# Optimization experiments

Measured on AMD Instinct MI355X. Metric: run time of the kernel, lower is better.

The kernel has to match this reference:

```python
import jax, jax.numpy as jnp
import numpy as np
from jax import lax

B, T, D, L, OUT, HORIZON, TSLOTS, NDAY = 512, 24, 1024, 2, 325, 12, 288, 7


def setup_inputs() -> dict:
    key = jax.random.key(0)
    ks = jax.random.split(key, 20)
    s_d = 1.0 / np.sqrt(D)
    s_o = 1.0 / np.sqrt(OUT)
    inp = {
        'data': jax.random.normal(ks[0], (B, T, OUT), jnp.float32),
        'time': jax.random.randint(ks[1], (B, T), 0, TSLOTS),
        'weekday': jax.random.randint(ks[2], (B,), 0, NDAY),
        # embedding params
        'w_data': jax.random.normal(ks[3], (OUT, D), jnp.float32) * s_o,
        'b_data': jnp.zeros((D,), jnp.float32),
        'time_table': jax.random.normal(ks[4], (TSLOTS, D), jnp.float32) * 0.02,
        'day_table': jax.random.normal(ks[5], (NDAY, D), jnp.float32) * 0.02,
        # encoder GRU (input_size == hidden_size == D for all layers)
        'enc_Wih': jax.random.uniform(ks[6], (L, 3 * D, D), jnp.float32, -s_d, s_d),
        'enc_Whh': jax.random.uniform(ks[7], (L, 3 * D, D), jnp.float32, -s_d, s_d),
        'enc_bih': jax.random.uniform(ks[8], (L, 3 * D), jnp.float32, -s_d, s_d),
        'enc_bhh': jax.random.uniform(ks[9], (L, 3 * D), jnp.float32, -s_d, s_d),
        # decoder GRU
        'dec_Wih': jax.random.uniform(ks[10], (L, 3 * D, D), jnp.float32, -s_d, s_d),
        'dec_Whh': jax.random.uniform(ks[11], (L, 3 * D, D), jnp.float32, -s_d, s_d),
        'dec_bih': jax.random.uniform(ks[12], (L, 3 * D), jnp.float32, -s_d, s_d),
        'dec_bhh': jax.random.uniform(ks[13], (L, 3 * D), jnp.float32, -s_d, s_d),
        # decoder output MLP (dropout=0 -> linear)
        'w_mlp': jax.random.uniform(ks[14], (D, OUT), jnp.float32, -s_d, s_d),
        'b_mlp': jnp.zeros((OUT,), jnp.float32),
    }
    return inp


def _gru_cell(h, x, Wih, Whh, bih, bhh):
    # torch GRUCell math. h,x: [B,D]
    gx = x @ Wih.T + bih            # [B,3D]
    gh = h @ Whh.T + bhh
    xr, xz, xn = jnp.split(gx, 3, axis=-1)
    hr, hz, hn = jnp.split(gh, 3, axis=-1)
    r = jax.nn.sigmoid(xr + hr)
    z = jax.nn.sigmoid(xz + hz)
    n = jnp.tanh(xn + r * hn)
    return (1.0 - z) * n + z * h


def _gru_layer(x, h0, Wih, Whh, bih, bhh):
    # x: [B,S,D] -> outputs [B,S,D], final h [B,D]
    def step(h, xt):
        h2 = _gru_cell(h, xt, Wih, Whh, bih, bhh)
        return h2, h2
    hT, ys = lax.scan(step, h0, jnp.moveaxis(x, 1, 0))
    return jnp.moveaxis(ys, 0, 1), hT


def reference(data, time, weekday, w_data, b_data, time_table, day_table,
              enc_Wih, enc_Whh, enc_bih, enc_bhh,
              dec_Wih, dec_Whh, dec_bih, dec_bhh, w_mlp, b_mlp):
    def embed(d, t, wd):  # d:[B,S,OUT] t:[B,S] wd:[B]
        return (d @ w_data + b_data
                + time_table[t % TSLOTS]
                + day_table[wd][:, None, :])

    # ---- encoder over history (all but last step) ----
    x = embed(data[:, :-1], time[:, :-1], weekday)  # [B,T-1,D]
    h_layers = []
    for l in range(L):
        x, hl = _gru_layer(x, jnp.zeros((B, D), x.dtype),
                           enc_Wih[l], enc_Whh[l], enc_bih[l], enc_bhh[l])
        h_layers.append(hl)
    hidden = jnp.stack(h_layers)  # [L,B,D]

    def dec_step(carry, _):
        hidden, data_i, time_i = carry  # [L,B,D], [B,1,OUT], [B,1]
        xi = embed(data_i, time_i, weekday)[:, 0]  # [B,D]
        new_h = []
        h_in = xi
        for l in range(L):
            hl = _gru_cell(hidden[l], h_in, dec_Wih[l], dec_Whh[l],
                           dec_bih[l], dec_bhh[l])
            new_h.append(hl)
            h_in = hl
        res = h_in @ w_mlp + b_mlp              # [B,OUT]
        out_i = data_i[:, 0] + res
        data_next = data_i[:, 0] + lax.stop_gradient(res)
        return (jnp.stack(new_h), data_next[:, None], time_i + 1), out_i

    carry0 = (hidden, data[:, -1:], time[:, -1:])
    _, outs = lax.scan(dec_step, carry0, None, length=HORIZON)  # [H,B,OUT]
    return jnp.moveaxis(outs, 0, 1)  # [B,H,OUT]
```

## Files before the change

### kernel.cpp

```cpp
#include <hip/hip_runtime.h>
#include <math.h>

#define B_ 512
#define T_ 24
#define TM1 23
#define D_ 1024
#define OUT_ 325
#define HORIZON_ 12

typedef unsigned short ushort_t;
typedef __attribute__((ext_vector_type(8))) short bf16x8;
typedef __attribute__((ext_vector_type(4))) float f32x4;

#define MFMA16(a, b, c) __builtin_amdgcn_mfma_f32_16x16x32_bf16((a), (b), (c), 0, 0, 0)

__device__ __forceinline__ ushort_t f2b(float f) {
  union { float f; unsigned u; } v; v.f = f;
  unsigned r = (v.u + 0x7fffu + ((v.u >> 16) & 1u)) >> 16;
  return (ushort_t)r;
}
__device__ __forceinline__ float b2f(ushort_t s) {
  union { unsigned u; float f; } v; v.u = ((unsigned)s) << 16;
  return v.f;
}

__device__ __forceinline__ size_t pidx16(int m, int k, int K) {
  return (((size_t)(m >> 4) * (K >> 5) + (k >> 5)) * 64
          + ((m & 15) + (((k >> 3) & 3) << 4))) * 8 + (k & 7);
}

#define GLOAD16(src, dst) \
  __builtin_amdgcn_global_load_lds((const __attribute__((address_space(1))) void*)(src), \
                                   (__attribute__((address_space(3))) void*)(dst), 16, 0, 0)

__global__ __launch_bounds__(256) void enc_diag(
    int k,
    const ushort_t* __restrict__ Hp0, const float* __restrict__ Hf0,
    float* __restrict__ Hf0o, ushort_t* __restrict__ Hp0o,
    const ushort_t* __restrict__ Whh0, const float* __restrict__ bhh0,
    const ushort_t* __restrict__ GXbuf, ushort_t* __restrict__ Y0p,
    const ushort_t* __restrict__ Hp1, const float* __restrict__ Hf1,
    float* __restrict__ Hf1o, ushort_t* __restrict__ Hp1o,
    const ushort_t* __restrict__ Wih1, const ushort_t* __restrict__ Whh1,
    const float* __restrict__ bih1, const float* __restrict__ bhh1)
{
  __shared__ ushort_t lds[2][16 * 512];
  const int tid = threadIdx.x, lane = tid & 63, w = tid >> 6;
  const int bid = blockIdx.x;
  const int z = bid >> 9, bx = (bid >> 5) & 15, by = bid & 31;
  const int wm = w >> 1, wn = w & 1;
  const int d = by * 32 + wn * 16 + (lane & 15);

  if (z == 0) {
    if (k >= TM1) return;
    const ushort_t* GXslot = GXbuf + (size_t)k * 512 * 3072;
    ushort_t* Seqp = Y0p + (size_t)k * 512 * 1024;
    f32x4 acc[3] = {};
    auto stage = [&](int buf, int kb) {
      #pragma unroll
      for (int r = 0; r < 2; ++r) {
        int s = w * 2 + r;
        const ushort_t* src;
        if (s < 2) src = Hp0 + ((size_t)(((bx * 32 + s * 16) >> 4) * 32 + kb)) * 512 + lane * 8;
        else { int g = (s - 2) >> 1, hf = (s - 2) & 1;
          src = Whh0 + ((size_t)((g * 64 + by * 2 + hf) * 32 + kb)) * 512 + lane * 8; }
        GLOAD16(src, &lds[buf][s * 512 + lane * 8]);
      }
    };
    stage(0, 0); __syncthreads();
    int cur = 0;
    for (int kb = 0; kb < 32; ++kb) {
      if (kb + 1 < 32) stage(cur ^ 1, kb + 1);
      const ushort_t* L = lds[cur];
      bf16x8 a = *(const bf16x8*)(L + wm * 512 + lane * 8);
      #pragma unroll
      for (int g = 0; g < 3; ++g) {
        bf16x8 b = *(const bf16x8*)(L + (2 + g * 2 + wn) * 512 + lane * 8);
        acc[g] = MFMA16(a, b, acc[g]);
      }
      __syncthreads(); cur ^= 1;
    }
    const float bh_r = bhh0[d], bh_z = bhh0[D_ + d], bh_n = bhh0[2 * D_ + d];
    #pragma unroll
    for (int q = 0; q < 4; ++q) {
      int m = bx * 32 + wm * 16 + ((lane >> 4) << 2) + q;
      const ushort_t* gxp = GXslot + (size_t)m * 3072 + d;
      float gx_r = b2f(gxp[0]), gx_z = b2f(gxp[D_]), gx_n = b2f(gxp[2 * D_]);
      float rr = 1.f / (1.f + __expf(-(gx_r + acc[0][q] + bh_r)));
      float zz = 1.f / (1.f + __expf(-(gx_z + acc[1][q] + bh_z)));
      float nn = tanhf(gx_n + rr * (acc[2][q] + bh_n));
      float h = Hf0[(size_t)m * D_ + d];
      float hnew = (1.f - zz) * nn + zz * h;
      Hf0o[(size_t)m * D_ + d] = hnew;
      ushort_t hb = f2b(hnew);
      size_t pi = pidx16(m, d, D_);
      Hp0o[pi] = hb; Seqp[pi] = hb;
    }
  } else {
    if (k < 1) return;
    const ushort_t* Xp_ = Y0p + (size_t)(k - 1) * 512 * 1024;
    f32x4 accx[3] = {}, acch[3] = {};
    auto stage = [&](int buf, int kb) {
      #pragma unroll
      for (int r = 0; r < 4; ++r) {
        int s = w * 4 + r;
        const ushort_t* src;
        if (s < 2) src = Xp_ + ((size_t)(((bx * 32 + s * 16) >> 4) * 32 + kb)) * 512 + lane * 8;
        else if (s < 4) src = Hp1 + ((size_t)(((bx * 32 + (s - 2) * 16) >> 4) * 32 + kb)) * 512 + lane * 8;
        else if (s < 10) { int g = (s - 4) >> 1, hf = (s - 4) & 1;
          src = Wih1 + ((size_t)((g * 64 + by * 2 + hf) * 32 + kb)) * 512 + lane * 8; }
        else { int g = (s - 10) >> 1, hf = (s - 10) & 1;
          src = Whh1 + ((size_t)((g * 64 + by * 2 + hf) * 32 + kb)) * 512 + lane * 8; }
        GLOAD16(src, &lds[buf][s * 512 + lane * 8]);
      }
    };
    stage(0, 0); __syncthreads();
    int cur = 0;
    for (int kb = 0; kb < 32; ++kb) {
      if (kb + 1 < 32) stage(cur ^ 1, kb + 1);
      const ushort_t* L = lds[cur];
      bf16x8 ax = *(const bf16x8*)(L + (0 + wm) * 512 + lane * 8);
      bf16x8 ah = *(const bf16x8*)(L + (2 + wm) * 512 + lane * 8);
      #pragma unroll
      for (int g = 0; g < 3; ++g) {
        bf16x8 bxw = *(const bf16x8*)(L + (4 + g * 2 + wn) * 512 + lane * 8);
        bf16x8 bhw = *(const bf16x8*)(L + (10 + g * 2 + wn) * 512 + lane * 8);
        accx[g] = MFMA16(ax, bxw, accx[g]);
        acch[g] = MFMA16(ah, bhw, acch[g]);
      }
      __syncthreads(); cur ^= 1;
    }
    const float bi_r = bih1[d], bi_z = bih1[D_ + d], bi_n = bih1[2 * D_ + d];
    const float bh_r = bhh1[d], bh_z = bhh1[D_ + d], bh_n = bhh1[2 * D_ + d];
    #pragma unroll
    for (int q = 0; q < 4; ++q) {
      int m = bx * 32 + wm * 16 + ((lane >> 4) << 2) + q;
      float rr = 1.f / (1.f + __expf(-(accx[0][q] + bi_r + acch[0][q] + bh_r)));
      float zz = 1.f / (1.f + __expf(-(accx[1][q] + bi_z + acch[1][q] + bh_z)));
      float nn = tanhf(accx[2][q] + bi_n + rr * (acch[2][q] + bh_n));
      float h = Hf1[(size_t)m * D_ + d];
      float hnew = (1.f - zz) * nn + zz * h;
      Hf1o[(size_t)m * D_ + d] = hnew;
      Hp1o[pidx16(m, d, D_)] = f2b(hnew);
    }
  }
}

__global__ __launch_bounds__(256) void dec_cell0(
    const ushort_t* __restrict__ DCp, const ushort_t* __restrict__ Hp,
    const float* __restrict__ Hf,
    const ushort_t* __restrict__ W0dp, const ushort_t* __restrict__ Whh0,
    const float* __restrict__ bhh0,
    const float* __restrict__ CTt, const float* __restrict__ CBd,
    const int* __restrict__ timev, int step,
    float* __restrict__ Hf_out, ushort_t* __restrict__ Hp_out)
{
  __shared__ ushort_t lds[2][16 * 512];
  const int tid = threadIdx.x, lane = tid & 63, w = tid >> 6;
  const int bid = blockIdx.x;
  const int bx = bid >> 5, by = bid & 31;
  const int wm = w >> 1, wn = w & 1;
  const int d = by * 32 + wn * 16 + (lane & 15);
  f32x4 accx[3] = {}, acch[3] = {};

  auto stage_h = [&](int buf, int kb) {
    #pragma unroll
    for (int r = 0; r < 2; ++r) {
      int s = (w == 0) ? (2 + r) : (8 + w * 2 + r);
      const ushort_t* src;
      if (s < 4) src = Hp + ((size_t)(((bx * 32 + (s - 2) * 16) >> 4) * 32 + kb)) * 512 + lane * 8;
      else { int g = (s - 10) >> 1, hf = (s - 10) & 1;
        src = Whh0 + ((size_t)((g * 64 + by * 2 + hf) * 32 + kb)) * 512 + lane * 8; }
      GLOAD16(src, &lds[buf][s * 512 + lane * 8]);
    }
  };
  auto stage_x = [&](int buf, int kb) {
    #pragma unroll
    for (int r = 0; r < 2; ++r) {
      int s = (w == 0) ? r : (2 + w * 2 + r);
      const ushort_t* src;
      if (s < 2) src = DCp + ((size_t)(((bx * 32 + s * 16) >> 4) * 11 + kb)) * 512 + lane * 8;
      else { int g = (s - 4) >> 1, hf = (s - 4) & 1;
        src = W0dp + ((size_t)((g * 64 + by * 2 + hf) * 11 + kb)) * 512 + lane * 8; }
      GLOAD16(src, &lds[buf][s * 512 + lane * 8]);
    }
  };

  stage_h(0, 0); stage_x(0, 0);
  __syncthreads();
  int cur = 0;
  for (int kb = 0; kb < 32; ++kb) {
    if (kb + 1 < 32) {
      stage_h(cur ^ 1, kb + 1);
      if (kb + 1 < 11) stage_x(cur ^ 1, kb + 1);
    }
    const ushort_t* L = lds[cur];
    bf16x8 ah = *(const bf16x8*)(L + (2 + wm) * 512 + lane * 8);
    if (kb < 11) {
      bf16x8 ax = *(const bf16x8*)(L + (0 + wm) * 512 + lane * 8);
      #pragma unroll
      for (int g = 0; g < 3; ++g) {
        bf16x8 bxw = *(const bf16x8*)(L + (4 + g * 2 + wn) * 512 + lane * 8);
        accx[g] = MFMA16(ax, bxw, accx[g]);
      }
    }
    #pragma unroll
    for (int g = 0; g < 3; ++g) {
      bf16x8 bhw = *(const bf16x8*)(L + (10 + g * 2 + wn) * 512 + lane * 8);
      acch[g] = MFMA16(ah, bhw, acch[g]);
    }
    __syncthreads(); cur ^= 1;
  }

  const float bh_r = bhh0[d], bh_z = bhh0[D_ + d], bh_n = bhh0[2 * D_ + d];
  #pragma unroll
  for (int q = 0; q < 4; ++q) {
    int m = bx * 32 + wm * 16 + ((lane >> 4) << 2) + q;
    int ti = (timev[m * T_ + (T_ - 1)] + step) % 288;
    const float* ctt = CTt + (size_t)ti * 3072;
    const float* cb  = CBd + (size_t)m * 3072;
    float gx_r = accx[0][q] + ctt[d] + cb[d];
    float gx_z = accx[1][q] + ctt[D_ + d] + cb[D_ + d];
    float gx_n = accx[2][q] + ctt[2 * D_ + d] + cb[2 * D_ + d];
    float rr = 1.f / (1.f + __expf(-(gx_r + acch[0][q] + bh_r)));
    float zz = 1.f / (1.f + __expf(-(gx_z + acch[1][q] + bh_z)));
    float nn = tanhf(gx_n + rr * (acch[2][q] + bh_n));
    float h = Hf[(size_t)m * D_ + d];
    float hnew = (1.f - zz) * nn + zz * h;
    Hf_out[(size_t)m * D_ + d] = hnew;
    Hp_out[pidx16(m, d, D_)] = f2b(hnew);
  }
}

__global__ __launch_bounds__(256) void gru_cell32(
    const ushort_t* __restrict__ Xp_, const ushort_t* __restrict__ Hp,
    const float* __restrict__ Hf,
    const ushort_t* __restrict__ Wih_l, const ushort_t* __restrict__ Whh_l,
    const float* __restrict__ bih_l, const float* __restrict__ bhh_l,
    float* __restrict__ Hf_out, ushort_t* __restrict__ Hp_out)
{
  __shared__ ushort_t lds[2][16 * 512];
  const int tid = threadIdx.x, lane = tid & 63, w = tid >> 6;
  const int bid = blockIdx.x;
  const int bx = bid >> 5, by = bid & 31;
  const int wm = w >> 1, wn = w & 1;
  const int d = by * 32 + wn * 16 + (lane & 15);
  f32x4 accx[3] = {}, acch[3] = {};

  auto stage = [&](int buf, int kb) {
    #pragma unroll
    for (int r = 0; r < 4; ++r) {
      int s = w * 4 + r;
      const ushort_t* src;
      if (s < 2) src = Xp_ + ((size_t)(((bx * 32 + s * 16) >> 4) * 32 + kb)) * 512 + lane * 8;
      else if (s < 4) src = Hp + ((size_t)(((bx * 32 + (s - 2) * 16) >> 4) * 32 + kb)) * 512 + lane * 8;
      else if (s < 10) { int g = (s - 4) >> 1, hf = (s - 4) & 1;
        src = Wih_l + ((size_t)((g * 64 + by * 2 + hf) * 32 + kb)) * 512 + lane * 8; }
      else { int g = (s - 10) >> 1, hf = (s - 10) & 1;
        src = Whh_l + ((size_t)((g * 64 + by * 2 + hf) * 32 + kb)) * 512 + lane * 8; }
      GLOAD16(src, &lds[buf][s * 512 + lane * 8]);
    }
  };

  stage(0, 0); __syncthreads();
  int cur = 0;
  for (int kb = 0; kb < 32; ++kb) {
    if (kb + 1 < 32) stage(cur ^ 1, kb + 1);
    const ushort_t* L = lds[cur];
    bf16x8 ax = *(const bf16x8*)(L + (0 + wm) * 512 + lane * 8);
    bf16x8 ah = *(const bf16x8*)(L + (2 + wm) * 512 + lane * 8);
    #pragma unroll
    for (int g = 0; g < 3; ++g) {
      bf16x8 bxw = *(const bf16x8*)(L + (4 + g * 2 + wn) * 512 + lane * 8);
      bf16x8 bhw = *(const bf16x8*)(L + (10 + g * 2 + wn) * 512 + lane * 8);
      accx[g] = MFMA16(ax, bxw, accx[g]);
      acch[g] = MFMA16(ah, bhw, acch[g]);
    }
    __syncthreads(); cur ^= 1;
  }

  const float bi_r = bih_l[d], bi_z = bih_l[D_ + d], bi_n = bih_l[2 * D_ + d];
  const float bh_r = bhh_l[d], bh_z = bhh_l[D_ + d], bh_n = bhh_l[2 * D_ + d];
  #pragma unroll
  for (int q = 0; q < 4; ++q) {
    int m = bx * 32 + wm * 16 + ((lane >> 4) << 2) + q;
    float rr = 1.f / (1.f + __expf(-(accx[0][q] + bi_r + acch[0][q] + bh_r)));
    float zz = 1.f / (1.f + __expf(-(accx[1][q] + bi_z + acch[1][q] + bh_z)));
    float nn = tanhf(accx[2][q] + bi_n + rr * (acch[2][q] + bh_n));
    float h = Hf[(size_t)m * D_ + d];
    float hnew = (1.f - zz) * nn + zz * h;
    Hf_out[(size_t)m * D_ + d] = hnew;
    Hp_out[pidx16(m, d, D_)] = f2b(hnew);
  }
}

__global__ __launch_bounds__(256) void gemm_gx0_enc(
    const ushort_t* __restrict__ Ap, const ushort_t* __restrict__ W0p,
    const float* __restrict__ CTt, const float* __restrict__ CBe,
    const int* __restrict__ timev,
    ushort_t* __restrict__ GX)
{
  __shared__ ushort_t lds[2][16 * 512];
  const int tid = threadIdx.x, lane = tid & 63, w = tid >> 6;
  const int bx = blockIdx.x, by = blockIdx.y;
  const int wm = w >> 1, wn = w & 1;
  f32x4 acc[4][4] = {};

  auto stage = [&](int buf, int kb) {
    #pragma unroll
    for (int r = 0; r < 4; ++r) {
      int s = r * 4 + w;
      const ushort_t* src = (s < 8)
          ? Ap  + ((size_t)((bx * 8 + s) * 11 + kb)) * 512 + lane * 8
          : W0p + ((size_t)((by * 8 + (s - 8)) * 11 + kb)) * 512 + lane * 8;
      GLOAD16(src, &lds[buf][s * 512 + lane * 8]);
    }
  };

  stage(0, 0); __syncthreads();
  int cur = 0;
  for (int kb = 0; kb < 11; ++kb) {
    if (kb + 1 < 11) stage(cur ^ 1, kb + 1);
    const ushort_t* L = lds[cur];
    bf16x8 af[4], bf[4];
    #pragma unroll
    for (int f = 0; f < 4; ++f) {
      af[f] = *(const bf16x8*)(L + (wm * 4 + f) * 512 + lane * 8);
      bf[f] = *(const bf16x8*)(L + (8 + wn * 4 + f) * 512 + lane * 8);
    }
    #pragma unroll
    for (int fm = 0; fm < 4; ++fm)
      #pragma unroll
      for (int fn = 0; fn < 4; ++fn)
        acc[fm][fn] = MFMA16(af[fm], bf[fn], acc[fm][fn]);
    __syncthreads(); cur ^= 1;
  }

  float* fl = (float*)&lds[0][0];
  for (int fm = 0; fm < 4; ++fm) {
    #pragma unroll
    for (int q = 0; q < 4; ++q)
      #pragma unroll
      for (int fn = 0; fn < 4; ++fn)
        fl[(wm * 16 + ((lane >> 4) << 2) + q) * 132 + wn * 64 + fn * 16 + (lane & 15)]
            = acc[fm][fn][q];
    __syncthreads();
    #pragma unroll
    for (int it = 0; it < 2; ++it) {
      int idx = it * 256 + tid;
      int ml = idx >> 4, n0 = (idx & 15) * 8;
      int m = bx * 128 + (ml >> 4) * 64 + fm * 16 + (ml & 15);
      int b = m / 23, t = m - b * 23;
      int ti = timev[b * T_ + t] % 288;
      const float* ctt = CTt + (size_t)ti * 3072 + by * 128 + n0;
      const float* cb  = CBe + (size_t)b * 3072 + by * 128 + n0;
      const float* fr  = fl + ml * 132 + n0;
      bf16x8 o;
      #pragma unroll
      for (int j = 0; j < 8; ++j) o[j] = f2b(fr[j] + ctt[j] + cb[j]);
      *(bf16x8*)(GX + ((size_t)t * 512 + b) * 3072 + by * 128 + n0) = o;
    }
    __syncthreads();
  }
}

template<int EPI>
__global__ __launch_bounds__(256) void gemm64(
    const ushort_t* __restrict__ Ap, const ushort_t* __restrict__ Wp, int K32,
    const float* __restrict__ bias, int step,
    ushort_t* __restrict__ outp, float* __restrict__ outf,
    float* __restrict__ dout, ushort_t* __restrict__ DCp)
{
  __shared__ ushort_t lds[2][8 * 512];
  const int tid = threadIdx.x, lane = tid & 63, w = tid >> 6;
  const int bx = blockIdx.x, by = blockIdx.y;
  const int wm = w >> 1, wn = w & 1;
  f32x4 acc[2][2] = {};

  auto stage = [&](int buf, int kb) {
    #pragma unroll
    for (int r = 0; r < 2; ++r) {
      int s = r * 4 + w;
      const ushort_t* src = (s < 4)
          ? Ap + ((size_t)((bx * 4 + s) * K32 + kb)) * 512 + lane * 8
          : Wp + ((size_t)((by * 4 + (s - 4)) * K32 + kb)) * 512 + lane * 8;
      GLOAD16(src, &lds[buf][s * 512 + lane * 8]);
    }
  };

  stage(0, 0); __syncthreads();
  int cur = 0;
  for (int kb = 0; kb < K32; ++kb) {
    if (kb + 1 < K32) stage(cur ^ 1, kb + 1);
    const ushort_t* L = lds[cur];
    bf16x8 af[2], bf[2];
    #pragma unroll
    for (int f = 0; f < 2; ++f) {
      af[f] = *(const bf16x8*)(L + (wm * 2 + f) * 512 + lane * 8);
      bf[f] = *(const bf16x8*)(L + (4 + wn * 2 + f) * 512 + lane * 8);
    }
    #pragma unroll
    for (int fm = 0; fm < 2; ++fm)
      #pragma unroll
      for (int fn = 0; fn < 2; ++fn)
        acc[fm][fn] = MFMA16(af[fm], bf[fn], acc[fm][fn]);
    __syncthreads(); cur ^= 1;
  }

  #pragma unroll
  for (int fm = 0; fm < 2; ++fm) {
    #pragma unroll
    for (int q = 0; q < 4; ++q) {
      int m = bx * 64 + wm * 32 + fm * 16 + ((lane >> 4) << 2) + q;
      #pragma unroll
      for (int fn = 0; fn < 2; ++fn) {
        int n = by * 64 + wn * 32 + fn * 16 + (lane & 15);
        float v = acc[fm][fn][q];
        if (EPI == 0) {
          if (n < 352) outp[pidx16(m, n, 352)] = f2b(v);
        } else if (EPI == 1) {
          outf[(size_t)m * 3072 + n] = v;
        } else {
          if (n < OUT_) {
            v += bias[n] + outf[(size_t)m * OUT_ + n];
            dout[((size_t)m * HORIZON_ + step) * OUT_ + n] = v;
            outf[(size_t)m * OUT_ + n] = v;
            DCp[pidx16(m, n, 352)] = f2b(v);
          }
        }
      }
    }
  }
}

__global__ void build_cb(const float* __restrict__ CT, const float* __restrict__ bih0,
                         const int* __restrict__ weekday, float* __restrict__ CB)
{
  int idx = blockIdx.x * 256 + threadIdx.x;
  if (idx >= 512 * 3072) return;
  int b = idx / 3072, n = idx - b * 3072;
  CB[idx] = CT[(size_t)(288 + weekday[b]) * 3072 + n] + CT[(size_t)295 * 3072 + n] + bih0[n];
}

__global__ void pack_k1024(const float* __restrict__ src, ushort_t* __restrict__ dst,
                           int total, int Mvalid) {
  int stride = gridDim.x * 256;
  for (int i = blockIdx.x * 256 + threadIdx.x; i < total; i += stride) {
    int seg = i >> 6, q = i & 63;
    int m = (seg >> 5) * 16 + (q & 15);
    int k = (seg & 31) * 32 + (q >> 4) * 8;
    bf16x8 o;
    if (m < Mvalid) {
      const float* s = src + (size_t)m * 1024 + k;
      float4 v0 = *(const float4*)s, v1 = *(const float4*)(s + 4);
      o[0] = f2b(v0.x); o[1] = f2b(v0.y); o[2] = f2b(v0.z); o[3] = f2b(v0.w);
      o[4] = f2b(v1.x); o[5] = f2b(v1.y); o[6] = f2b(v1.z); o[7] = f2b(v1.w);
    } else o = bf16x8{0,0,0,0,0,0,0,0};
    *(bf16x8*)(dst + (size_t)i * 8) = o;
  }
}
__global__ void pack_wm(const float* __restrict__ w_mlp, ushort_t* __restrict__ dst) {
  int stride = gridDim.x * 256;
  for (int i = blockIdx.x * 256 + threadIdx.x; i < 384 * 128; i += stride) {
    int seg = i >> 6, q = i & 63;
    int n = (seg >> 5) * 16 + (q & 15);
    int k = (seg & 31) * 32 + (q >> 4) * 8;
    bf16x8 o;
    #pragma unroll
    for (int j = 0; j < 8; ++j)
      o[j] = (n < OUT_) ? f2b(w_mlp[(size_t)(k + j) * OUT_ + n]) : (short)0;
    *(bf16x8*)(dst + (size_t)i * 8) = o;
  }
}
__global__ void pack_ct(const float* __restrict__ time_table, const float* __restrict__ day_table,
                        const float* __restrict__ b_data, ushort_t* __restrict__ dst) {
  int stride = gridDim.x * 256;
  for (int i = blockIdx.x * 256 + threadIdx.x; i < 320 * 128; i += stride) {
    int seg = i >> 6, q = i & 63;
    int r = (seg >> 5) * 16 + (q & 15);
    int k = (seg & 31) * 32 + (q >> 4) * 8;
    const float* s = nullptr;
    if (r < 288) s = time_table + (size_t)r * 1024 + k;
    else if (r < 295) s = day_table + (size_t)(r - 288) * 1024 + k;
    else if (r == 295) s = b_data + k;
    bf16x8 o;
    #pragma unroll
    for (int j = 0; j < 8; ++j) o[j] = s ? f2b(s[j]) : (short)0;
    *(bf16x8*)(dst + (size_t)i * 8) = o;
  }
}
__global__ void pack_ae(const float* __restrict__ data, ushort_t* __restrict__ Ap) {
  int stride = gridDim.x * 256;
  const int total = (11776 / 16) * 11 * 64;
  for (int i = blockIdx.x * 256 + threadIdx.x; i < total; i += stride) {
    int seg = i >> 6, q = i & 63;
    int m = (seg / 11) * 16 + (q & 15);
    int k = (seg % 11) * 32 + (q >> 4) * 8;
    int b = m / TM1, t = m - b * TM1;
    const float* s = data + ((size_t)b * T_ + t) * OUT_;
    bf16x8 o;
    #pragma unroll
    for (int j = 0; j < 8; ++j) {
      int kk = k + j;
      o[j] = (kk < OUT_) ? f2b(s[kk]) : (short)0;
    }
    *(bf16x8*)(Ap + (size_t)i * 8) = o;
  }
}
__global__ void pack_dc(const float* __restrict__ data, ushort_t* __restrict__ DCp,
                        float* __restrict__ DC) {
  int stride = gridDim.x * 256;
  const int total = (512 / 16) * 11 * 64;
  for (int i = blockIdx.x * 256 + threadIdx.x; i < total; i += stride) {
    int seg = i >> 6, q = i & 63;
    int b = (seg / 11) * 16 + (q & 15);
    int k = (seg % 11) * 32 + (q >> 4) * 8;
    const float* s = data + ((size_t)b * T_ + (T_ - 1)) * OUT_;
    bf16x8 o;
    #pragma unroll
    for (int j = 0; j < 8; ++j) {
      int kk = k + j;
      float v = (kk < OUT_) ? s[kk] : 0.f;
      o[j] = f2b(v);
      if (kk < OUT_) DC[(size_t)b * OUT_ + kk] = v;
    }
    *(bf16x8*)(DCp + (size_t)i * 8) = o;
  }
}

extern "C" void kernel_launch(void* const* d_in, const int* in_sizes, int n_in,
                              void* d_out, int out_size, void* d_ws, size_t ws_size,
                              hipStream_t stream) {
  const float* data       = (const float*)d_in[0];
  const int*   timev      = (const int*)  d_in[1];
  const int*   weekday    = (const int*)  d_in[2];
  const float* w_data     = (const float*)d_in[3];
  const float* b_data     = (const float*)d_in[4];
  const float* time_table = (const float*)d_in[5];
  const float* day_table  = (const float*)d_in[6];
  const float* enc_Wih    = (const float*)d_in[7];
  const float* enc_Whh    = (const float*)d_in[8];
  const float* enc_bih    = (const float*)d_in[9];
  const float* enc_bhh    = (const float*)d_in[10];
  const float* dec_Wih    = (const float*)d_in[11];
  const float* dec_Whh    = (const float*)d_in[12];
  const float* dec_bih    = (const float*)d_in[13];
  const float* dec_bhh    = (const float*)d_in[14];
  const float* w_mlp      = (const float*)d_in[15];
  const float* b_mlp      = (const float*)d_in[16];
  float* out = (float*)d_out;

  char* base = (char*)d_ws;
  size_t o = 0;
  auto take = [&](size_t bytes) { void* p = base + o; o = (o + bytes + 511) & ~(size_t)511; return p; };
  const size_t WSZ = (size_t)6144 * 1024 * 2;
  ushort_t* Wih_e = (ushort_t*)take(WSZ);
  ushort_t* Whh_e = (ushort_t*)take(WSZ);
  ushort_t* Wih_d = (ushort_t*)take(WSZ);
  ushort_t* Whh_d = (ushort_t*)take(WSZ);
  ushort_t* WdTk  = (ushort_t*)take((size_t)384 * 1024 * 2);
  ushort_t* WmT   = (ushort_t*)take((size_t)384 * 1024 * 2);
  ushort_t* CTpk  = (ushort_t*)take((size_t)320 * 1024 * 2);
  ushort_t* W0ep  = (ushort_t*)take((size_t)3072 * 352 * 2);
  ushort_t* W0dp  = (ushort_t*)take((size_t)3072 * 352 * 2);
  float*    CTe   = (float*)take((size_t)320 * 3072 * 4);
  float*    CTd   = (float*)take((size_t)320 * 3072 * 4);
  float*    CBe   = (float*)take((size_t)512 * 3072 * 4);
  float*    CBd   = (float*)take((size_t)512 * 3072 * 4);
  ushort_t* Ap    = (ushort_t*)take((size_t)11776 * 352 * 2);
  ushort_t* Xp    = (ushort_t*)take((size_t)23 * 512 * 1024 * 2);
  ushort_t* GXbuf = (ushort_t*)take((size_t)23 * 512 * 3072 * 2);
  ushort_t* DCp   = (ushort_t*)take((size_t)512 * 352 * 2);
  float*    DC    = (float*)take((size_t)512 * OUT_ * 4);
  float*    Hfb   = (float*)take((size_t)4 * 512 * 1024 * 4 + (size_t)4 * 512 * 1024 * 2);
  if (o > ws_size) return;

  float* Hf0[2], *Hf1[2]; ushort_t* Hp0[2], *Hp1[2];
  ushort_t* Hpb = (ushort_t*)(Hfb + (size_t)4 * 512 * 1024);
  for (int p = 0; p < 2; ++p) {
    Hf0[p] = Hfb + (size_t)p * 512 * 1024;
    Hf1[p] = Hfb + (size_t)(2 + p) * 512 * 1024;
    Hp0[p] = Hpb + (size_t)p * 512 * 1024;
    Hp1[p] = Hpb + (size_t)(2 + p) * 512 * 1024;
  }

  const size_t WLAYER = (size_t)3072 * 1024;

  pack_k1024<<<3072, 256, 0, stream>>>(enc_Wih, Wih_e, 6144 * 128, 6144);
  pack_k1024<<<3072, 256, 0, stream>>>(enc_Whh, Whh_e, 6144 * 128, 6144);
  pack_k1024<<<3072, 256, 0, stream>>>(dec_Wih, Wih_d, 6144 * 128, 6144);
  pack_k1024<<<3072, 256, 0, stream>>>(dec_Whh, Whh_d, 6144 * 128, 6144);
  pack_k1024<<<192, 256, 0, stream>>>(w_data, WdTk, 384 * 128, OUT_);
  pack_wm<<<192, 256, 0, stream>>>(w_mlp, WmT);
  pack_ct<<<160, 256, 0, stream>>>(time_table, day_table, b_data, CTpk);
  pack_ae<<<2048, 256, 0, stream>>>(data, Ap);
  pack_dc<<<88, 256, 0, stream>>>(data, DCp, DC);

  gemm64<0><<<dim3(48, 6), 256, 0, stream>>>(Wih_e, WdTk, 32, nullptr, 0, W0ep, nullptr, nullptr, nullptr);
  gemm64<0><<<dim3(48, 6), 256, 0, stream>>>(Wih_d, WdTk, 32, nullptr, 0, W0dp, nullptr, nullptr, nullptr);
  gemm64<1><<<dim3(5, 48), 256, 0, stream>>>(CTpk, Wih_e, 32, nullptr, 0, nullptr, CTe, nullptr, nullptr);
  gemm64<1><<<dim3(5, 48), 256, 0, stream>>>(CTpk, Wih_d, 32, nullptr, 0, nullptr, CTd, nullptr, nullptr);
  build_cb<<<6144, 256, 0, stream>>>(CTe, enc_bih, weekday, CBe);
  build_cb<<<6144, 256, 0, stream>>>(CTd, dec_bih, weekday, CBd);

  gemm_gx0_enc<<<dim3(92, 24), 256, 0, stream>>>(Ap, W0ep, CTe, CBe, timev, GXbuf);

  hipMemsetAsync(Hf0[0], 0, (size_t)512 * 1024 * 4, stream);
  hipMemsetAsync(Hf1[0], 0, (size_t)512 * 1024 * 4, stream);
  hipMemsetAsync(Hp0[0], 0, (size_t)512 * 1024 * 2, stream);
  hipMemsetAsync(Hp1[0], 0, (size_t)512 * 1024 * 2, stream);

  int p0 = 0, p1 = 0;
  for (int k = 0; k <= TM1; ++k) {
    enc_diag<<<1024, 256, 0, stream>>>(k,
        Hp0[p0], Hf0[p0], Hf0[1 - p0], Hp0[1 - p0], Whh_e, enc_bhh, GXbuf, Xp,
        Hp1[p1], Hf1[p1], Hf1[1 - p1], Hp1[1 - p1],
        Wih_e + WLAYER, Whh_e + WLAYER, enc_bih + 3072, enc_bhh + 3072);
    if (k < TM1) p0 ^= 1;
    if (k >= 1)  p1 ^= 1;
  }

  for (int s = 0; s < HORIZON_; ++s) {
    dec_cell0<<<512, 256, 0, stream>>>(
        DCp, Hp0[p0], Hf0[p0], W0dp, Whh_d, dec_bhh, CTd, CBd, timev, s,
        Hf0[1 - p0], Hp0[1 - p0]);
    p0 ^= 1;
    gru_cell32<<<512, 256, 0, stream>>>(
        Hp0[p0], Hp1[p1], Hf1[p1],
        Wih_d + WLAYER, Whh_d + WLAYER, dec_bih + 3072, dec_bhh + 3072,
        Hf1[1 - p1], Hp1[1 - p1]);
    p1 ^= 1;
    gemm64<3><<<dim3(8, 6), 256, 0, stream>>>(
        Hp1[p1], WmT, 32, b_mlp, s, nullptr, DC, out, DCp);
  }
}
```

Before: 1.453 ms.

## Triple-buffer LDS staging with explicit vmcnt waits and single barrier per K-step

Converts the double-buffered global_load_lds pipelines in the encoder, decoder and GRU cell kernels to three buffers with prefetch distance two. Each iteration waits on vmcnt for only the oldest stage and uses one barrier instead of a trailing __syncthreads. dec_cell0 is also restructured to stream the hidden GEMM and then the input GEMM as one 43-step sequence over a smaller LDS tile, so no iteration is half-empty. This aims to hide more global load latency and cut sync overhead, at the cost of more LDS per block and reliance on hand-counted vmcnt values.

Measured after the change: 1.561 ms. +7.4%, slower.

```diff
diff --git a/kernel.cpp b/kernel.cpp
--- a/kernel.cpp
+++ b/kernel.cpp
@@ -32,6 +32,11 @@
 #define GLOAD16(src, dst) \
   __builtin_amdgcn_global_load_lds((const __attribute__((address_space(1))) void*)(src), \
                                    (__attribute__((address_space(3))) void*)(dst), 16, 0, 0)
+
+#define WAITV2() asm volatile("s_waitcnt vmcnt(2)" ::: "memory")
+#define WAITV4() asm volatile("s_waitcnt vmcnt(4)" ::: "memory")
+#define WAITV0() asm volatile("s_waitcnt vmcnt(0)" ::: "memory")
+#define BARRIER_() { __builtin_amdgcn_s_barrier(); __builtin_amdgcn_sched_barrier(0); }
 
 __global__ __launch_bounds__(256) void enc_diag(
     int k,
@@ -44,7 +49,7 @@
     const ushort_t* __restrict__ Wih1, const ushort_t* __restrict__ Whh1,
     const float* __restrict__ bih1, const float* __restrict__ bhh1)
 {
-  __shared__ ushort_t lds[2][16 * 512];
+  __shared__ ushort_t lds[3][16 * 512];
   const int tid = threadIdx.x, lane = tid & 63, w = tid >> 6;
   const int bid = blockIdx.x;
   const int z = bid >> 9, bx = (bid >> 5) & 15, by = bid & 31;
@@ -67,18 +72,18 @@
         GLOAD16(src, &lds[buf][s * 512 + lane * 8]);
       }
     };
-    stage(0, 0); __syncthreads();
-    int cur = 0;
+    stage(0, 0); stage(1, 1);
     for (int kb = 0; kb < 32; ++kb) {
-      if (kb + 1 < 32) stage(cur ^ 1, kb + 1);
-      const ushort_t* L = lds[cur];
+      if (kb < 31) { WAITV2(); } else { WAITV0(); }
+      BARRIER_();
+      if (kb + 2 < 32) stage((kb + 2) % 3, kb + 2);
+      const ushort_t* L = lds[kb % 3];
       bf16x8 a = *(const bf16x8*)(L + wm * 512 + lane * 8);
       #pragma unroll
       for (int g = 0; g < 3; ++g) {
         bf16x8 b = *(const bf16x8*)(L + (2 + g * 2 + wn) * 512 + lane * 8);
         acc[g] = MFMA16(a, b, acc[g]);
       }
-      __syncthreads(); cur ^= 1;
     }
     const float bh_r = bhh0[d], bh_z = bhh0[D_ + d], bh_n = bhh0[2 * D_ + d];
     #pragma unroll
@@ -114,11 +119,12 @@
         GLOAD16(src, &lds[buf][s * 512 + lane * 8]);
       }
     };
-    stage(0, 0); __syncthreads();
-    int cur = 0;
+    stage(0, 0); stage(1, 1);
     for (int kb = 0; kb < 32; ++kb) {
-      if (kb + 1 < 32) stage(cur ^ 1, kb + 1);
-      const ushort_t* L = lds[cur];
+      if (kb < 31) { WAITV4(); } else { WAITV0(); }
+      BARRIER_();
+      if (kb + 2 < 32) stage((kb + 2) % 3, kb + 2);
+      const ushort_t* L = lds[kb % 3];
       bf16x8 ax = *(const bf16x8*)(L + (0 + wm) * 512 + lane * 8);
       bf16x8 ah = *(const bf16x8*)(L + (2 + wm) * 512 + lane * 8);
       #pragma unroll
@@ -128,7 +134,6 @@
         accx[g] = MFMA16(ax, bxw, accx[g]);
         acch[g] = MFMA16(ah, bhw, acch[g]);
       }
-      __syncthreads(); cur ^= 1;
     }
     const float bi_r = bih1[d], bi_z = bih1[D_ + d], bi_n = bih1[2 * D_ + d];
     const float bh_r = bhh1[d], bh_z = bhh1[D_ + d], bh_n = bhh1[2 * D_ + d];
@@ -155,61 +160,54 @@
     const int* __restrict__ timev, int step,
     float* __restrict__ Hf_out, ushort_t* __restrict__ Hp_out)
 {
-  __shared__ ushort_t lds[2][16 * 512];
+  __shared__ ushort_t lds[3][8 * 512];
   const int tid = threadIdx.x, lane = tid & 63, w = tid >> 6;
   const int bid = blockIdx.x;
   const int bx = bid >> 5, by = bid & 31;
   const int wm = w >> 1, wn = w & 1;
   const int d = by * 32 + wn * 16 + (lane & 15);
   f32x4 accx[3] = {}, acch[3] = {};
-
-  auto stage_h = [&](int buf, int kb) {
+  const int NT = 43;
+
+  auto stage = [&](int buf, int j) {
     #pragma unroll
     for (int r = 0; r < 2; ++r) {
-      int s = (w == 0) ? (2 + r) : (8 + w * 2 + r);
+      int s = w * 2 + r;
       const ushort_t* src;
-      if (s < 4) src = Hp + ((size_t)(((bx * 32 + (s - 2) * 16) >> 4) * 32 + kb)) * 512 + lane * 8;
-      else { int g = (s - 10) >> 1, hf = (s - 10) & 1;
-        src = Whh0 + ((size_t)((g * 64 + by * 2 + hf) * 32 + kb)) * 512 + lane * 8; }
+      if (j < 32) {
+        if (s < 2) src = Hp + ((size_t)(((bx * 32 + s * 16) >> 4) * 32 + j)) * 512 + lane * 8;
+        else { int g = (s - 2) >> 1, hf = (s - 2) & 1;
+          src = Whh0 + ((size_t)((g * 64 + by * 2 + hf) * 32 + j)) * 512 + lane * 8; }
+      } else {
+        int jj = j - 32;
+        if (s < 2) src = DCp + ((size_t)(((bx * 32 + s * 16) >> 4) * 11 + jj)) * 512 + lane * 8;
+        else { int g = (s - 2) >> 1, hf = (s - 2) & 1;
+          src = W0dp + ((size_t)((g * 64 + by * 2 + hf) * 11 + jj)) * 512 + lane * 8; }
+      }
       GLOAD16(src, &lds[buf][s * 512 + lane * 8]);
     }
   };
-  auto stage_x = [&](int buf, int kb) {
-    #pragma unroll
-    for (int r = 0; r < 2; ++r) {
-      int s = (w == 0) ? r : (2 + w * 2 + r);
-      const ushort_t* src;
-      if (s < 2) src = DCp + ((size_t)(((bx * 32 + s * 16) >> 4) * 11 + kb)) * 512 + lane * 8;
-      else { int g = (s - 4) >> 1, hf = (s - 4) & 1;
-        src = W0dp + ((size_t)((g * 64 + by * 2 + hf) * 11 + kb)) * 512 + lane * 8; }
-      GLOAD16(src, &lds[buf][s * 512 + lane * 8]);
-    }
-  };
-
-  stage_h(0, 0); stage_x(0, 0);
-  __syncthreads();
-  int cur = 0;
-  for (int kb = 0; kb < 32; ++kb) {
-    if (kb + 1 < 32) {
-      stage_h(cur ^ 1, kb + 1);
-      if (kb + 1 < 11) stage_x(cur ^ 1, kb + 1);
-    }
-    const ushort_t* L = lds[cur];
-    bf16x8 ah = *(const bf16x8*)(L + (2 + wm) * 512 + lane * 8);
-    if (kb < 11) {
-      bf16x8 ax = *(const bf16x8*)(L + (0 + wm) * 512 + lane * 8);
+
+  stage(0, 0); stage(1, 1);
+  for (int j = 0; j < NT; ++j) {
+    if (j < NT - 1) { WAITV2(); } else { WAITV0(); }
+    BARRIER_();
+    if (j + 2 < NT) stage((j + 2) % 3, j + 2);
+    const ushort_t* L = lds[j % 3];
+    bf16x8 a = *(const bf16x8*)(L + wm * 512 + lane * 8);
+    if (j < 32) {
       #pragma unroll
       for (int g = 0; g < 3; ++g) {
-        bf16x8 bxw = *(const bf16x8*)(L + (4 + g * 2 + wn) * 512 + lane * 8);
-        accx[g] = MFMA16(ax, bxw, accx[g]);
-      }
-    }
-    #pragma unroll
-    for (int g = 0; g < 3; ++g) {
-      bf16x8 bhw = *(const bf16x8*)(L + (10 + g * 2 + wn) * 512 + lane * 8);
-      acch[g] = MFMA16(ah, bhw, acch[g]);
-    }
-    __syncthreads(); cur ^= 1;
+        bf16x8 b = *(const bf16x8*)(L + (2 + g * 2 + wn) * 512 + lane * 8);
+        acch[g] = MFMA16(a, b, acch[g]);
+      }
+    } else {
+      #pragma unroll
+      for (int g = 0; g < 3; ++g) {
+        bf16x8 b = *(const bf16x8*)(L + (2 + g * 2 + wn) * 512 + lane * 8);
+        accx[g] = MFMA16(a, b, accx[g]);
+      }
+    }
   }
 
   const float bh_r = bhh0[d], bh_z = bhh0[D_ + d], bh_n = bhh0[2 * D_ + d];
@@ -239,7 +237,7 @@
     const float* __restrict__ bih_l, const float* __restrict__ bhh_l,
     float* __restrict__ Hf_out, ushort_t* __restrict__ Hp_out)
 {
-  __shared__ ushort_t lds[2][16 * 512];
+  __shared__ ushort_t lds[3][16 * 512];
   const int tid = threadIdx.x, lane = tid & 63, w = tid >> 6;
   const int bid = blockIdx.x;
   const int bx = bid >> 5, by = bid & 31;
@@ -262,11 +260,12 @@
     }
   };
 
-  stage(0, 0); __syncthreads();
-  int cur = 0;
+  stage(0, 0); stage(1, 1);
   for (int kb = 0; kb < 32; ++kb) {
-    if (kb + 1 < 32) stage(cur ^ 1, kb + 1);
-    const ushort_t* L = lds[cur];
+    if (kb < 31) { WAITV4(); } else { WAITV0(); }
+    BARRIER_();
+    if (kb + 2 < 32) stage((kb + 2) % 3, kb + 2);
+    const ushort_t* L = lds[kb % 3];
     bf16x8 ax = *(const bf16x8*)(L + (0 + wm) * 512 + lane * 8);
     bf16x8 ah = *(const bf16x8*)(L + (2 + wm) * 512 + lane * 8);
     #pragma unroll
@@ -276,7 +275,6 @@
       accx[g] = MFMA16(ax, bxw, accx[g]);
       acch[g] = MFMA16(ah, bhw, acch[g]);
     }
-    __syncthreads(); cur ^= 1;
   }
 
   const float bi_r = bih_l[d], bi_z = bih_l[D_ + d], bi_n = bih_l[2 * D_ + d];
```

## Split layer-1 encoder GEMM into separate input-projection stage in wavefront pipeline

Applied to the files above, without the earlier changes.

The encoder wavefront goes from a two-stage to a three-stage diagonal schedule. Layer-1's input projection (Y0 @ Wih1) now runs in its own block group and writes bf16 gates to a double-buffered GX1p buffer. The layer-1 recurrent blocks then read those gates one step later and do only the Whh1 GEMM. This balances per-block work (every block does a single K=1024 GEMM with half the LDS) and raises the grid to 1536 blocks. The cost is one extra launch, an extra bf16 round trip for the gates, and added rounding error in the layer-1 input gates.

Result: faster. 1.405 ms (-3.3%).

```diff
diff --git a/kernel.cpp b/kernel.cpp
--- a/kernel.cpp
+++ b/kernel.cpp
@@ -39,110 +39,101 @@
     float* __restrict__ Hf0o, ushort_t* __restrict__ Hp0o,
     const ushort_t* __restrict__ Whh0, const float* __restrict__ bhh0,
     const ushort_t* __restrict__ GXbuf, ushort_t* __restrict__ Y0p,
+    const ushort_t* __restrict__ Wih1, const float* __restrict__ bih1,
+    ushort_t* __restrict__ GX1p,
     const ushort_t* __restrict__ Hp1, const float* __restrict__ Hf1,
     float* __restrict__ Hf1o, ushort_t* __restrict__ Hp1o,
-    const ushort_t* __restrict__ Wih1, const ushort_t* __restrict__ Whh1,
-    const float* __restrict__ bih1, const float* __restrict__ bhh1)
+    const ushort_t* __restrict__ Whh1, const float* __restrict__ bhh1)
 {
-  __shared__ ushort_t lds[2][16 * 512];
+  __shared__ ushort_t lds[2][8 * 512];
   const int tid = threadIdx.x, lane = tid & 63, w = tid >> 6;
   const int bid = blockIdx.x;
   const int z = bid >> 9, bx = (bid >> 5) & 15, by = bid & 31;
   const int wm = w >> 1, wn = w & 1;
   const int d = by * 32 + wn * 16 + (lane & 15);
 
+  const ushort_t *Abase, *Bbase;
   if (z == 0) {
     if (k >= TM1) return;
-    const ushort_t* GXslot = GXbuf + (size_t)k * 512 * 3072;
-    ushort_t* Seqp = Y0p + (size_t)k * 512 * 1024;
-    f32x4 acc[3] = {};
-    auto stage = [&](int buf, int kb) {
-      #pragma unroll
-      for (int r = 0; r < 2; ++r) {
-        int s = w * 2 + r;
-        const ushort_t* src;
-        if (s < 2) src = Hp0 + ((size_t)(((bx * 32 + s * 16) >> 4) * 32 + kb)) * 512 + lane * 8;
-        else { int g = (s - 2) >> 1, hf = (s - 2) & 1;
-          src = Whh0 + ((size_t)((g * 64 + by * 2 + hf) * 32 + kb)) * 512 + lane * 8; }
-        GLOAD16(src, &lds[buf][s * 512 + lane * 8]);
-      }
-    };
-    stage(0, 0); __syncthreads();
-    int cur = 0;
-    for (int kb = 0; kb < 32; ++kb) {
-      if (kb + 1 < 32) stage(cur ^ 1, kb + 1);
-      const ushort_t* L = lds[cur];
-      bf16x8 a = *(const bf16x8*)(L + wm * 512 + lane * 8);
+    Abase = Hp0; Bbase = Whh0;
+  } else if (z == 1) {
+    if (k < 1 || k > TM1) return;
+    Abase = Y0p + (size_t)(k - 1) * 512 * 1024; Bbase = Wih1;
+  } else {
+    if (k < 2) return;
+    Abase = Hp1; Bbase = Whh1;
+  }
+
+  f32x4 acc[3] = {};
+  auto stage = [&](int buf, int kb) {
+    #pragma unroll
+    for (int r = 0; r < 2; ++r) {
+      int s = w * 2 + r;
+      const ushort_t* src;
+      if (s < 2) src = Abase + ((size_t)(((bx * 32 + s * 16) >> 4) * 32 + kb)) * 512 + lane * 8;
+      else { int g = (s - 2) >> 1, hf = (s - 2) & 1;
+        src = Bbase + ((size_t)((g * 64 + by * 2 + hf) * 32 + kb)) * 512 + lane * 8; }
+      GLOAD16(src, &lds[buf][s * 512 + lane * 8]);
+    }
+  };
+  stage(0, 0); __syncthreads();
+  int cur = 0;
+  for (int kb = 0; kb < 32; ++kb) {
+    if (kb + 1 < 32) stage(cur ^ 1, kb + 1);
+    const ushort_t* L = lds[cur];
+    bf16x8 a = *(const bf16x8*)(L + wm * 512 + lane * 8);
+    #pragma unroll
+    for (int g = 0; g < 3; ++g) {
+      bf16x8 b = *(const bf16x8*)(L + (2 + g * 2 + wn) * 512 + lane * 8);
+      acc[g] = MFMA16(a, b, acc[g]);
+    }
+    __syncthreads(); cur ^= 1;
+  }
+
+  if (z == 1) {
+    ushort_t* G = GX1p + (size_t)((k - 1) & 1) * 512 * 3072;
+    #pragma unroll
+    for (int q = 0; q < 4; ++q) {
+      int m = bx * 32 + wm * 16 + ((lane >> 4) << 2) + q;
       #pragma unroll
       for (int g = 0; g < 3; ++g) {
-        bf16x8 b = *(const bf16x8*)(L + (2 + g * 2 + wn) * 512 + lane * 8);
-        acc[g] = MFMA16(a, b, acc[g]);
+        int n = g * 1024 + d;
+        G[pidx16(m, n, 3072)] = f2b(acc[g][q] + bih1[n]);
       }
-      __syncthreads(); cur ^= 1;
-    }
-    const float bh_r = bhh0[d], bh_z = bhh0[D_ + d], bh_n = bhh0[2 * D_ + d];
-    #pragma unroll
-    for (int q = 0; q < 4; ++q) {
-      int m = bx * 32 + wm * 16 + ((lane >> 4) << 2) + q;
-      const ushort_t* gxp = GXslot + (size_t)m * 3072 + d;
-      float gx_r = b2f(gxp[0]), gx_z = b2f(gxp[D_]), gx_n = b2f(gxp[2 * D_]);
-      float rr = 1.f / (1.f + __expf(-(gx_r + acc[0][q] + bh_r)));
-      float zz = 1.f / (1.f + __expf(-(gx_z + acc[1][q] + bh_z)));
-      float nn = tanhf(gx_n + rr * (acc[2][q] + bh_n));
-      float h = Hf0[(size_t)m * D_ + d];
-      float hnew = (1.f - zz) * nn + zz * h;
-      Hf0o[(size_t)m * D_ + d] = hnew;
-      ushort_t hb = f2b(hnew);
-      size_t pi = pidx16(m, d, D_);
-      Hp0o[pi] = hb; Seqp[pi] = hb;
-    }
-  } else {
-    if (k < 1) return;
-    const ushort_t* Xp_ = Y0p + (size_t)(k - 1) * 512 * 1024;
-    f32x4 accx[3] = {}, acch[3] = {};
-    auto stage = [&](int buf, int kb) {
-      #pragma unroll
-      for (int r = 0; r < 4; ++r) {
-        int s = w * 4 + r;
-        const ushort_t* src;
-        if (s < 2) src = Xp_ + ((size_t)(((bx * 32 + s * 16) >> 4) * 32 + kb)) * 512 + lane * 8;
-        else if (s < 4) src = Hp1 + ((size_t)(((bx * 32 + (s - 2) * 16) >> 4) * 32 + kb)) * 512 + lane * 8;
-        else if (s < 10) { int g = (s - 4) >> 1, hf = (s - 4) & 1;
-          src = Wih1 + ((size_t)((g * 64 + by * 2 + hf) * 32 + kb)) * 512 + lane * 8; }
-        else { int g = (s - 10) >> 1, hf = (s - 10) & 1;
-          src = Whh1 + ((size_t)((g * 64 + by * 2 + hf) * 32 + kb)) * 512 + lane * 8; }
-        GLOAD16(src, &lds[buf][s * 512 + lane * 8]);
-      }
-    };
-    stage(0, 0); __syncthreads();
-    int cur = 0;
-    for (int kb = 0; kb < 32; ++kb) {
-      if (kb + 1 < 32) stage(cur ^ 1, kb + 1);
-      const ushort_t* L = lds[cur];
-      bf16x8 ax = *(const bf16x8*)(L + (0 + wm) * 512 + lane * 8);
-      bf16x8 ah = *(const bf16x8*)(L + (2 + wm) * 512 + lane * 8);
-      #pragma unroll
-      for (int g = 0; g < 3; ++g) {
-        bf16x8 bxw = *(const bf16x8*)(L + (4 + g * 2 + wn) * 512 + lane * 8);
-        bf16x8 bhw = *(const bf16x8*)(L + (10 + g * 2 + wn) * 512 + lane * 8);
-        accx[g] = MFMA16(ax, bxw, accx[g]);
-        acch[g] = MFMA16(ah, bhw, acch[g]);
-      }
-      __syncthreads(); cur ^= 1;
-    }
-    const float bi_r = bih1[d], bi_z = bih1[D_ + d], bi_n = bih1[2 * D_ + d];
-    const float bh_r = bhh1[d], bh_z = bhh1[D_ + d], bh_n = bhh1[2 * D_ + d];
-    #pragma unroll
-    for (int q = 0; q < 4; ++q) {
-      int m = bx * 32 + wm * 16 + ((lane >> 4) << 2) + q;
-      float rr = 1.f / (1.f + __expf(-(accx[0][q] + bi_r + acch[0][q] + bh_r)));
-      float zz = 1.f / (1.f + __expf(-(accx[1][q] + bi_z + acch[1][q] + bh_z)));
-      float nn = tanhf(accx[2][q] + bi_n + rr * (acch[2][q] + bh_n));
-      float h = Hf1[(size_t)m * D_ + d];
-      float hnew = (1.f - zz) * nn + zz * h;
-      Hf1o[(size_t)m * D_ + d] = hnew;
-      Hp1o[pidx16(m, d, D_)] = f2b(hnew);
-    }
+    }
+    return;
+  }
+
+  const float* bhh = (z == 0) ? bhh0 : bhh1;
+  const float* Hf  = (z == 0) ? Hf0 : Hf1;
+  float* HfO       = (z == 0) ? Hf0o : Hf1o;
+  ushort_t* HpO    = (z == 0) ? Hp0o : Hp1o;
+  const float bh_r = bhh[d], bh_z = bhh[D_ + d], bh_n = bhh[2 * D_ + d];
+  const ushort_t* GXrow = (z == 0) ? (GXbuf + (size_t)k * 512 * 3072) : nullptr;
+  const ushort_t* G2 = (z == 2) ? (GX1p + (size_t)(k & 1) * 512 * 3072) : nullptr;
+  ushort_t* Seqp = (z == 0) ? (Y0p + (size_t)k * 512 * 1024) : nullptr;
+  #pragma unroll
+  for (int q = 0; q < 4; ++q) {
+    int m = bx * 32 + wm * 16 + ((lane >> 4) << 2) + q;
+    float gx_r, gx_z, gx_n;
+    if (z == 0) {
+      const ushort_t* gxp = GXrow + (size_t)m * 3072 + d;
+      gx_r = b2f(gxp[0]); gx_z = b2f(gxp[D_]); gx_n = b2f(gxp[2 * D_]);
+    } else {
+      gx_r = b2f(G2[pidx16(m, d, 3072)]);
+      gx_z = b2f(G2[pidx16(m, D_ + d, 3072)]);
+      gx_n = b2f(G2[pidx16(m, 2 * D_ + d, 3072)]);
+    }
+    float rr = 1.f / (1.f + __expf(-(gx_r + acc[0][q] + bh_r)));
+    float zz = 1.f / (1.f + __expf(-(gx_z + acc[1][q] + bh_z)));
+    float nn = tanhf(gx_n + rr * (acc[2][q] + bh_n));
+    float h = Hf[(size_t)m * D_ + d];
+    float hnew = (1.f - zz) * nn + zz * h;
+    HfO[(size_t)m * D_ + d] = hnew;
+    ushort_t hb = f2b(hnew);
+    size_t pi = pidx16(m, d, D_);
+    HpO[pi] = hb;
+    if (z == 0) Seqp[pi] = hb;
   }
 }
 
@@ -570,6 +561,7 @@
   ushort_t* Ap    = (ushort_t*)take((size_t)11776 * 352 * 2);
   ushort_t* Xp    = (ushort_t*)take((size_t)23 * 512 * 1024 * 2);
   ushort_t* GXbuf = (ushort_t*)take((size_t)23 * 512 * 3072 * 2);
+  ushort_t* GX1p  = (ushort_t*)take((size_t)2 * 512 * 3072 * 2);
   ushort_t* DCp   = (ushort_t*)take((size_t)512 * 352 * 2);
   float*    DC    = (float*)take((size_t)512 * OUT_ * 4);
   float*    Hfb   = (float*)take((size_t)4 * 512 * 1024 * 4 + (size_t)4 * 512 * 1024 * 2);
@@ -611,13 +603,14 @@
   hipMemsetAsync(Hp1[0], 0, (size_t)512 * 1024 * 2, stream);
 
   int p0 = 0, p1 = 0;
-  for (int k = 0; k <= TM1; ++k) {
-    enc_diag<<<1024, 256, 0, stream>>>(k,
+  for (int k = 0; k <= TM1 + 1; ++k) {
+    enc_diag<<<1536, 256, 0, stream>>>(k,
         Hp0[p0], Hf0[p0], Hf0[1 - p0], Hp0[1 - p0], Whh_e, enc_bhh, GXbuf, Xp,
+        Wih_e + WLAYER, enc_bih + 3072, GX1p,
         Hp1[p1], Hf1[p1], Hf1[1 - p1], Hp1[1 - p1],
-        Wih_e + WLAYER, Whh_e + WLAYER, enc_bih + 3072, enc_bhh + 3072);
+        Whh_e + WLAYER, enc_bhh + 3072);
     if (k < TM1) p0 ^= 1;
-    if (k >= 1)  p1 ^= 1;
+    if (k >= 2)  p1 ^= 1;
   }
 
   for (int s = 0; s < HORIZON_; ++s) {
```
